# Optimization experiments

Hardware: AMD Instinct MI355X
Metric: run time of the kernel (lower is better)

The kernel has to match this reference:

```python
import jax, jax.numpy as jnp
import numpy as np

NPRE = 8        # diffusion iterations (production default 8000; math identical per step)
DEPS = 0.1
LAMBDA = 0.24
K_PM = 0.03     # exp(log(0.03)) buffer in the 'none' branch
ALPHA = 0.7
SIGMA_FREQ = 0.1


def _g_pm(x, K):
    # Perona-Malik conductance g(x) = 1 / (1 + |x^2| / K^2)
    return 1.0 / (1.0 + jnp.abs(x * x) / (K * K))


def _gaussian_blur3(x, sigma):
    # Replicates torch create_gaussian_kernel(3, sigma): linspace(-3//2, 3//2, 3) = [-2, -0.5, 1]
    xs = jnp.linspace(-2.0, 1.0, 3)
    g1 = jnp.exp(-(xs ** 2) / (2.0 * sigma * sigma))
    g1 = g1 / g1.sum()
    k2 = jnp.outer(g1, g1).astype(x.dtype)            # [3,3]
    C = x.shape[1]
    k = jnp.broadcast_to(k2, (C, 1, 3, 3))
    xp = jnp.pad(x, ((0, 0), (0, 0), (1, 1), (1, 1)), mode='reflect')
    return jax.lax.conv_general_dilated(
        xp, k, window_strides=(1, 1), padding='VALID',
        dimension_numbers=('NCHW', 'OIHW', 'NCHW'), feature_group_count=C)


def _edge_coeffs(I, K):
    # c(I): FFT high-pass edge response + finite differences -> Perona-Malik coefficients
    b, c_, h, w = I.shape
    F = jnp.fft.fft2(I, norm='ortho')
    y = jnp.linspace(-1.0, 1.0, h)[:, None]
    xg = jnp.linspace(-1.0, 1.0, w)[None, :]
    hf_mask = (jnp.sqrt(xg * xg + y * y) > 0.5).astype(I.dtype)   # [h,w]
    er = jnp.real(jnp.fft.ifft2(F * hf_mask, norm='ortho'))
    dv = jnp.abs(I[:, :, 1:, :] - I[:, :, :-1, :]) + er[:, :, 1:, :]
    dh = jnp.abs(I[:, :, :, 1:] - I[:, :, :, :-1]) + er[:, :, :, 1:]
    cv = _g_pm(jnp.mean(dv, axis=1, keepdims=True), K)   # [b,1,h-1,w]
    ch = _g_pm(jnp.mean(dh, axis=1, keepdims=True), K)   # [b,1,h,w-1]
    return cv, ch


def _diffuse_step(cv, ch, I, l=LAMBDA):
    # frequency-domain smoothing branch
    Ff = jnp.fft.fft2(I, norm='ortho')
    sr = _gaussian_blur3(jnp.real(Ff), SIGMA_FREQ)
    si = _gaussian_blur3(jnp.imag(Ff), SIGMA_FREQ)
    I_freq = jnp.real(jnp.fft.ifft2(jax.lax.complex(sr, si), norm='ortho'))
    dv = I[:, :, 1:, :] - I[:, :, :-1, :]
    dh = I[:, :, :, 1:] - I[:, :, :, :-1]
    I = ALPHA * I + (1.0 - ALPHA) * I_freq
    tv = l * cv * dv
    th = l * ch * dh
    I = I.at[:, :, 1:, :].add(-tv).at[:, :, :-1, :].add(tv)
    I = I.at[:, :, :, 1:].add(-th).at[:, :, :, :-1].add(th)
    return I


def _adjust_step(img, source, mask_inv, eps=1e-8):
    b, c_, h, w = img.shape
    sh, sw = source.shape[2], source.shape[3]
    fh, fw = h // sh, w // sw
    # AdaptiveAvgPool2d((sh,sw)) with integer factor == block mean
    img_ss = img.reshape(b, c_, sh, fh, sw, fw).mean(axis=(3, 5))
    ratio_ss = jnp.where(mask_inv, jnp.ones_like(img_ss), source / (img_ss + eps))
    # nearest upsample with integer factor == repeat
    ratio = jnp.repeat(jnp.repeat(ratio_ss, fh, axis=2), fw, axis=3)
    return img * ratio


def setup_inputs() -> dict:
    key = jax.random.key(0)
    k1, k2, k3, k4 = jax.random.split(key, 4)
    guide = jax.random.normal(k1, (4, 3, 1024, 1024), dtype=jnp.float32)
    source = jax.random.uniform(k2, (4, 1, 128, 128), dtype=jnp.float32)
    mask_lr = jax.random.uniform(k3, (4, 1, 128, 128), dtype=jnp.float32)
    y_bicubic = jax.random.uniform(k4, (4, 1, 1024, 1024), dtype=jnp.float32)
    return {"guide": guide, "source": source, "mask_lr": mask_lr, "y_bicubic": y_bicubic}


def reference(guide, source, mask_lr, y_bicubic):
    # depth shift when source.min() <= deps (uniform[0,1) source -> effectively always)
    shift = jnp.where(jnp.min(source) <= DEPS, DEPS, 0.0).astype(source.dtype)
    source = source + shift
    img = y_bicubic + shift
    mask_inv = mask_lr < 0.5

    # 'none' feature extractor: guide_feats = cat([guide, img], 1) -> [B,4,H,W]
    feats = jnp.concatenate([guide, img], axis=1)
    cv, ch = _edge_coeffs(feats, K_PM)

    def step(I, _):
        I = _diffuse_step(cv, ch, I)
        I = _adjust_step(I, source, mask_inv)
        return I, None

    img, _ = jax.lax.scan(step, img, None, length=NPRE)
    return img - shift
```

## Files before the change

kernel.cpp:

```cpp
#include <hip/hip_runtime.h>
#include <hip/hip_fp16.h>

namespace {

constexpr int H = 1024, W = 1024, NB = 4;
constexpr int SH = 128, SW = 128;
constexpr float LAM = 0.24f;
constexpr float KK = 0.03f * 0.03f;
constexpr float DEPS_V = 0.1f;
constexpr float FFT_SCALE = 1.0f / (1024.0f * 1024.0f);
constexpr int COL_LO = 256, NCOL = 512;

__device__ __forceinline__ float2 cadd(float2 a, float2 b) { return make_float2(a.x + b.x, a.y + b.y); }
__device__ __forceinline__ float2 csub(float2 a, float2 b) { return make_float2(a.x - b.x, a.y - b.y); }
__device__ __forceinline__ float2 cmul(float2 a, float2 b) {
  return make_float2(a.x * b.x - a.y * b.y, a.x * b.y + a.y * b.x);
}
__device__ __forceinline__ int phys2(int e) { return e + (e >> 4); }

__device__ __forceinline__ float shift_from_bits(const unsigned* minp) {
  float mn = __uint_as_float(minp[0]);
  return (mn <= DEPS_V) ? DEPS_V : 0.0f;
}

__global__ void k_shift_min(const float* __restrict__ src, unsigned* __restrict__ minp) {
  int t = threadIdx.x;
  int b0 = blockIdx.x * 1024;
  float m = fminf(fminf(src[b0 + t], src[b0 + t + 256]),
                  fminf(src[b0 + t + 512], src[b0 + t + 768]));
  for (int o = 32; o > 0; o >>= 1) m = fminf(m, __shfl_xor(m, o));
  __shared__ float sm[4];
  if ((t & 63) == 0) sm[t >> 6] = m;
  __syncthreads();
  if (t == 0) {
    float mm = fminf(fminf(sm[0], sm[1]), fminf(sm[2], sm[3]));
    atomicMin(minp, __float_as_uint(mm));
  }
}

template <int NS, bool INV>
__device__ __forceinline__ void r4_butterfly(float2 v[4], int j, float2 r[4]) {
  if (NS > 1) {
    int p = j & (NS - 1);
    float sn, cs;
    sincospif((INV ? 1.0f : -1.0f) * (float)p * (1.0f / (float)(2 * NS)), &sn, &cs);
    float2 w1 = make_float2(cs, sn);
    float2 w2 = cmul(w1, w1);
    float2 w3 = cmul(w2, w1);
    v[1] = cmul(v[1], w1);
    v[2] = cmul(v[2], w2);
    v[3] = cmul(v[3], w3);
  }
  float2 a0 = cadd(v[0], v[2]), a2 = csub(v[0], v[2]);
  float2 a1 = cadd(v[1], v[3]), a3 = csub(v[1], v[3]);
  a3 = INV ? make_float2(-a3.y, a3.x) : make_float2(a3.y, -a3.x);
  r[0] = cadd(a0, a1);
  r[2] = csub(a0, a1);
  r[1] = cadd(a2, a3);
  r[3] = csub(a2, a3);
}

template <int NS, bool INV>
__device__ __forceinline__ void r4_stage_lds(float2 v[4], float2* dst, int j) {
  float2 r[4];
  r4_butterfly<NS, INV>(v, j, r);
  int p = j & (NS - 1);
  int base = ((j - p) << 2) + p;
#pragma unroll
  for (int k = 0; k < 4; ++k) dst[phys2(base + k * NS)] = r[k];
}

__device__ __forceinline__ void lds_load4(const float2* src, float2 v[4], int j) {
#pragma unroll
  for (int k = 0; k < 4; ++k) v[k] = src[phys2(j + k * 256)];
}

template <bool INV>
__device__ void fft1024(float2 v[4], float2* b0, float2* b1, int j) {
  r4_stage_lds<1, INV>(v, b0, j);
  __syncthreads();
  lds_load4(b0, v, j);
  r4_stage_lds<4, INV>(v, b1, j);
  __syncthreads();
  lds_load4(b1, v, j);
  r4_stage_lds<16, INV>(v, b0, j);
  __syncthreads();
  lds_load4(b0, v, j);
  r4_stage_lds<64, INV>(v, b1, j);
  __syncthreads();
  lds_load4(b1, v, j);
  float2 r[4];
  r4_butterfly<256, INV>(v, j, r);
#pragma unroll
  for (int k = 0; k < 4; ++k) v[k] = r[k];
}

__global__ void k_rowfft_fwd(const float* __restrict__ guide, const float* __restrict__ ybic,
                             const unsigned* __restrict__ minp, float2* __restrict__ A) {
  __shared__ float2 b0[1088], b1[1088];
  int b = blockIdx.y, y0 = blockIdx.x * 2, j = threadIdx.x;
  float sh = shift_from_bits(minp);
  const float* g0 = guide + ((size_t)(b * 3 + 0) * H + y0) * W;
  const float* g1 = guide + ((size_t)(b * 3 + 1) * H + y0) * W;
  const float* g2 = guide + ((size_t)(b * 3 + 2) * H + y0) * W;
  const float* yb = ybic + ((size_t)b * H + y0) * W;
  float2 v[4];
#pragma unroll
  for (int k = 0; k < 4; ++k) {
    int x = j + k * 256;
    float s0 = g0[x] + g1[x] + g2[x] + (yb[x] + sh);
    float s1 = g0[x + W] + g1[x + W] + g2[x + W] + (yb[x + W] + sh);
    v[k] = make_float2(s0, s1);
  }
  fft1024<false>(v, b0, b1, j);
#pragma unroll
  for (int k = 0; k < 4; ++k) b0[phys2(j + k * 256)] = v[k];
  __syncthreads();
  float2* o0 = A + ((size_t)b * H + y0) * W;
  float2* o1 = o0 + W;
#pragma unroll
  for (int k = 0; k < 4; ++k) {
    int m = j + k * 256;
    float2 Zm = v[k];
    float2 Zc = b0[phys2((1024 - m) & 1023)];
    o0[m] = make_float2(0.5f * (Zm.x + Zc.x), 0.5f * (Zm.y - Zc.y));
    o1[m] = make_float2(0.5f * (Zm.y + Zc.y), 0.5f * (Zc.x - Zm.x));
  }
}

__global__ void k_transpose_fwd(const float2* __restrict__ A, float2* __restrict__ Bc) {
  __shared__ float2 tile[32][33];
  int b = blockIdx.z;
  int c0 = blockIdx.x * 32, y0 = blockIdx.y * 32;
  const float2* ip = A + (size_t)b * H * W;
  float2* op = Bc + (size_t)b * NCOL * H;
#pragma unroll
  for (int k = 0; k < 4; ++k)
    tile[threadIdx.y + k * 8][threadIdx.x] =
        ip[(size_t)(y0 + threadIdx.y + k * 8) * W + (COL_LO + c0 + threadIdx.x)];
  __syncthreads();
#pragma unroll
  for (int k = 0; k < 4; ++k)
    op[(size_t)(c0 + threadIdx.y + k * 8) * H + (y0 + threadIdx.x)] =
        tile[threadIdx.x][threadIdx.y + k * 8];
}

__global__ void k_transpose_bwd(const float2* __restrict__ Bc, float2* __restrict__ A) {
  __shared__ float2 tile[32][33];
  int b = blockIdx.z;
  int c0 = blockIdx.x * 32, y0 = blockIdx.y * 32;
  const float2* ip = Bc + (size_t)b * NCOL * H;
  float2* op = A + (size_t)b * H * W;
#pragma unroll
  for (int k = 0; k < 4; ++k)
    tile[threadIdx.y + k * 8][threadIdx.x] =
        ip[(size_t)(c0 + threadIdx.y + k * 8) * H + (y0 + threadIdx.x)];
  __syncthreads();
#pragma unroll
  for (int k = 0; k < 4; ++k)
    op[(size_t)(y0 + threadIdx.y + k * 8) * W + (COL_LO + c0 + threadIdx.x)] =
        tile[threadIdx.x][threadIdx.y + k * 8];
}

__global__ void k_colfft_mask(float2* __restrict__ Bc) {
  __shared__ float2 b0[1088], b1[1088];
  int b = blockIdx.y, r = blockIdx.x, j = threadIdx.x;
  int k2 = COL_LO + r;
  double xj = -1.0 + 2.0 * (double)k2 / 1023.0;
  double xj2 = xj * xj;
  float2* row = Bc + ((size_t)b * NCOL + r) * H;
  float2 v[4];
#pragma unroll
  for (int k = 0; k < 4; ++k) v[k] = row[j + k * 256];
  fft1024<false>(v, b0, b1, j);
#pragma unroll
  for (int k = 0; k < 4; ++k) {
    int i = j + k * 256;
    double yv = -1.0 + 2.0 * (double)i / 1023.0;
    if (xj2 + yv * yv <= 0.25) v[k] = make_float2(0.0f, 0.0f);
  }
  fft1024<true>(v, b0, b1, j);
#pragma unroll
  for (int k = 0; k < 4; ++k) row[j + k * 256] = v[k];
}

__global__ void k_rowfft_inv(const float2* __restrict__ A, float* __restrict__ er) {
  __shared__ float2 b0[1088], b1[1088];
  int b = blockIdx.y, y = blockIdx.x, j = threadIdx.x;
  const float2* in = A + ((size_t)b * H + y) * W;
  float2 v[4];
#pragma unroll
  for (int k = 0; k < 4; ++k) v[k] = in[j + k * 256];
  v[0].x *= 1024.0f; v[0].y *= 1024.0f;
  v[3].x *= 1024.0f; v[3].y *= 1024.0f;
  fft1024<true>(v, b0, b1, j);
  float* out = er + ((size_t)b * H + y) * W;
#pragma unroll
  for (int k = 0; k < 4; ++k) out[j + k * 256] = v[k].x * FFT_SCALE;
}

__global__ void k_coeffs(const float* __restrict__ guide, const float* __restrict__ ybic,
                         const float* __restrict__ er, __half2* __restrict__ cvh) {
  int b = blockIdx.y, y = blockIdx.x, t = threadIdx.x;
  int x0 = t * 4;
  const float* g = guide + (size_t)b * 3 * H * W;
  const float* yb = ybic + (size_t)b * H * W;
  const float* e = er + (size_t)b * H * W;
  __half2* cp = cvh + (size_t)b * H * W;
  const size_t CH = (size_t)H * W;
  size_t row = (size_t)y * W + x0;
  float4 a0 = *(const float4*)(g + row);
  float4 a1 = *(const float4*)(g + CH + row);
  float4 a2 = *(const float4*)(g + 2 * CH + row);
  float4 a3 = *(const float4*)(yb + row);
  float4 e0 = *(const float4*)(e + row);
  float A0[5] = {a0.x, a0.y, a0.z, a0.w, 0.f};
  float A1[5] = {a1.x, a1.y, a1.z, a1.w, 0.f};
  float A2[5] = {a2.x, a2.y, a2.z, a2.w, 0.f};
  float A3[5] = {a3.x, a3.y, a3.z, a3.w, 0.f};
  float E0[5] = {e0.x, e0.y, e0.z, e0.w, 0.f};
  bool hasR = (x0 + 4 < W);
  if (hasR) {
    A0[4] = g[row + 4]; A1[4] = g[CH + row + 4]; A2[4] = g[2 * CH + row + 4];
    A3[4] = yb[row + 4]; E0[4] = e[row + 4];
  }
  float B0[4], B1[4], B2[4], B3[4], E1[4];
  bool hasD = (y < H - 1);
  if (hasD) {
    float4 q0 = *(const float4*)(g + row + W);
    float4 q1 = *(const float4*)(g + CH + row + W);
    float4 q2 = *(const float4*)(g + 2 * CH + row + W);
    float4 q3 = *(const float4*)(yb + row + W);
    float4 q4 = *(const float4*)(e + row + W);
    B0[0]=q0.x; B0[1]=q0.y; B0[2]=q0.z; B0[3]=q0.w;
    B1[0]=q1.x; B1[1]=q1.y; B1[2]=q1.z; B1[3]=q1.w;
    B2[0]=q2.x; B2[1]=q2.y; B2[2]=q2.z; B2[3]=q2.w;
    B3[0]=q3.x; B3[1]=q3.y; B3[2]=q3.z; B3[3]=q3.w;
    E1[0]=q4.x; E1[1]=q4.y; E1[2]=q4.z; E1[3]=q4.w;
  }
  __half2 outq[4];
#pragma unroll
  for (int i = 0; i < 4; ++i) {
    float cvv = 0.0f;
    if (hasD) {
      float s = fabsf(B0[i] - A0[i]) + fabsf(B1[i] - A1[i]) +
                fabsf(B2[i] - A2[i]) + fabsf(B3[i] - A3[i]);
      s = (s + E1[i]) * 0.25f;
      cvv = 1.0f / (1.0f + (s * s) / KK);
    }
    float chv = 0.0f;
    if (i < 3 || hasR) {
      float s = fabsf(A0[i + 1] - A0[i]) + fabsf(A1[i + 1] - A1[i]) +
                fabsf(A2[i + 1] - A2[i]) + fabsf(A3[i + 1] - A3[i]);
      s = (s + E0[i + 1]) * 0.25f;
      chv = 1.0f / (1.0f + (s * s) / KK);
    }
    outq[i] = __floats2half2_rn(cvv, chv);
  }
  *(float4*)(cp + row) = *(const float4*)outq;
}

__device__ __forceinline__ void load8h(const __half* p, float o[8]) {
  float4 raw = *(const float4*)p;
  const __half2* h = (const __half2*)&raw;
#pragma unroll
  for (int i = 0; i < 4; ++i) {
    float2 f = __half22float2(h[i]);
    o[2 * i] = f.x; o[2 * i + 1] = f.y;
  }
}
__device__ __forceinline__ void load8f(const float* p, float o[8]) {
  float4 a = *(const float4*)p;
  float4 c = *(const float4*)(p + 4);
  o[0]=a.x; o[1]=a.y; o[2]=a.z; o[3]=a.w; o[4]=c.x; o[5]=c.y; o[6]=c.z; o[7]=c.w;
}
__device__ __forceinline__ void store8h(__half* p, const float o[8]) {
  float4 raw;
  __half2* h = (__half2*)&raw;
#pragma unroll
  for (int i = 0; i < 4; ++i) h[i] = __floats2half2_rn(o[2 * i], o[2 * i + 1]);
  *(float4*)p = raw;
}

template <bool FIRST, bool FINAL>
__global__ void k_diffuse_ratio(const float* __restrict__ inF, const __half* __restrict__ inH,
                                const float* __restrict__ ratio_in,
                                const unsigned* __restrict__ minp,
                                const __half2* __restrict__ cvh, const float* __restrict__ src,
                                const float* __restrict__ mask, float* __restrict__ outF,
                                __half* __restrict__ outH, float* __restrict__ ratio_out) {
  int b = blockIdx.z, tx = threadIdx.x, ty = threadIdx.y;
  int x0 = blockIdx.x * 256 + tx * 8;
  int y = blockIdx.y * 8 + ty;
  float sh = shift_from_bits(minp);
  float addv = FIRST ? sh : 0.0f;
  size_t base = (size_t)b * H * W;
  size_t row = (size_t)y * W + x0;
  bool hasU = (y > 0), hasD = (y < H - 1);
  bool hasL = (x0 > 0), hasR = (x0 + 8 < W);
  int px = x0 >> 3;
  float rq = 1.f, rup = 1.f, rdn = 1.f, rlf = 1.f, rrt = 1.f;
  if (!FIRST) {
    const float* rb = ratio_in + (size_t)b * SH * SW;
    int py = y >> 3;
    rq = rb[py * SW + px];
    rup = hasU ? rb[((y - 1) >> 3) * SW + px] : 1.f;
    rdn = hasD ? rb[((y + 1) >> 3) * SW + px] : 1.f;
    rlf = hasL ? rb[py * SW + (px - 1)] : 1.f;
    rrt = hasR ? rb[py * SW + (px + 1)] : 1.f;
  }
  float C[8], U[8] = {0}, D[8] = {0};
  float lf = 0.f, rt = 0.f;
  if (FIRST) {
    const float* I = inF + base;
    load8f(I + row, C);
    if (hasU) load8f(I + row - W, U);
    if (hasD) load8f(I + row + W, D);
    if (hasL) lf = I[row - 1];
    if (hasR) rt = I[row + 8];
  } else {
    const __half* I = inH + base;
    load8h(I + row, C);
    if (hasU) load8h(I + row - W, U);
    if (hasD) load8h(I + row + W, D);
    if (hasL) lf = __half2float(I[row - 1]);
    if (hasR) rt = __half2float(I[row + 8]);
  }
#pragma unroll
  for (int i = 0; i < 8; ++i) {
    C[i] = (C[i] + addv) * rq;
    U[i] = (U[i] + addv) * rup;
    D[i] = (D[i] + addv) * rdn;
  }
  lf = (lf + addv) * rlf;
  rt = (rt + addv) * rrt;
  const __half2* cp = cvh + base;
  float cvq[8], chq[8], cvu[8] = {0};
  {
    float4 r0 = *(const float4*)(cp + row);
    float4 r1 = *(const float4*)(cp + row + 4);
    const __half2* h0 = (const __half2*)&r0;
    const __half2* h1 = (const __half2*)&r1;
#pragma unroll
    for (int i = 0; i < 4; ++i) {
      float2 f = __half22float2(h0[i]); cvq[i] = f.x; chq[i] = f.y;
      float2 g = __half22float2(h1[i]); cvq[i + 4] = g.x; chq[i + 4] = g.y;
    }
    if (hasU) {
      float4 u0 = *(const float4*)(cp + row - W);
      float4 u1 = *(const float4*)(cp + row - W + 4);
      const __half2* p0 = (const __half2*)&u0;
      const __half2* p1 = (const __half2*)&u1;
#pragma unroll
      for (int i = 0; i < 4; ++i) {
        cvu[i] = __half2float(p0[i].x);
        cvu[i + 4] = __half2float(p1[i].x);
      }
    }
  }
  float chl = hasL ? __half2float(cp[row - 1].y) : 0.f;
  float acc[8];
#pragma unroll
  for (int i = 0; i < 8; ++i) {
    float L = (i == 0) ? lf : C[i - 1];
    float R = (i == 7) ? rt : C[i + 1];
    float cL = (i == 0) ? chl : chq[i - 1];
    float a = C[i];
    if (hasD) a += LAM * cvq[i] * (D[i] - C[i]);
    if (hasU) a -= LAM * cvu[i] * (C[i] - U[i]);
    if (i < 7 || hasR) a += LAM * chq[i] * (R - C[i]);
    if (i > 0 || hasL) a -= LAM * cL * (C[i] - L);
    acc[i] = a;
  }
  __shared__ float sd[8][32];
  __shared__ float rblk[32];
  sd[ty][tx] = acc[0] + acc[1] + acc[2] + acc[3] + acc[4] + acc[5] + acc[6] + acc[7];
  __syncthreads();
  if (ty == 0) {
    float s = 0.f;
#pragma unroll
    for (int r = 0; r < 8; ++r) s += sd[r][tx];
    size_t si = ((size_t)b * SH + blockIdx.y) * SW + (blockIdx.x * 32 + tx);
    float mean = s * (1.0f / 64.0f);
    float rv = (mask[si] < 0.5f) ? 1.0f : (src[si] + sh) / (mean + 1e-8f);
    if (FINAL) rblk[tx] = rv;
    else ratio_out[si] = rv;
  }
  if (FINAL) {
    __syncthreads();
    float rv = rblk[tx];
    float o[8];
#pragma unroll
    for (int i = 0; i < 8; ++i) o[i] = acc[i] * rv - sh;
    float* op = outF + base + row;
    *(float4*)op = make_float4(o[0], o[1], o[2], o[3]);
    *(float4*)(op + 4) = make_float4(o[4], o[5], o[6], o[7]);
  } else {
    store8h(outH + base + row, acc);
  }
}

}

extern "C" void kernel_launch(void* const* d_in, const int* in_sizes, int n_in, void* d_out,
                              int out_size, void* d_ws, size_t ws_size, hipStream_t stream) {
  (void)in_sizes; (void)n_in; (void)out_size; (void)ws_size;
  const float* guide = (const float*)d_in[0];
  const float* source = (const float*)d_in[1];
  const float* mask = (const float*)d_in[2];
  const float* ybic = (const float*)d_in[3];
  float* out = (float*)d_out;

  char* ws = (char*)d_ws;
  float2* A = (float2*)ws;
  float2* Bc = (float2*)(ws + (size_t)32 * 1024 * 1024);
  float* er = (float*)(ws + (size_t)32 * 1024 * 1024);
  __half2* cvh = (__half2*)(ws + (size_t)48 * 1024 * 1024);
  __half* hA = (__half*)ws;
  __half* hB = (__half*)(ws + (size_t)8 * 1024 * 1024);
  unsigned* minp = (unsigned*)(ws + (size_t)64 * 1024 * 1024);
  float* ratioA = (float*)(ws + (size_t)64 * 1024 * 1024 + 4096);
  float* ratioB = ratioA + (size_t)NB * SH * SW;

  k_shift_min<<<64, 256, 0, stream>>>(source, minp);

  k_rowfft_fwd<<<dim3(H / 2, NB), 256, 0, stream>>>(guide, ybic, minp, A);
  dim3 gT(NCOL / 32, H / 32, NB), bT(32, 8);
  k_transpose_fwd<<<gT, bT, 0, stream>>>(A, Bc);
  k_colfft_mask<<<dim3(NCOL, NB), 256, 0, stream>>>(Bc);
  k_transpose_bwd<<<gT, bT, 0, stream>>>(Bc, A);
  k_rowfft_inv<<<dim3(H, NB), 256, 0, stream>>>(A, er);

  k_coeffs<<<dim3(H, NB), 256, 0, stream>>>(guide, ybic, er, cvh);

  dim3 gD(W / 256, H / 8, NB), bD(32, 8);
  k_diffuse_ratio<true, false><<<gD, bD, 0, stream>>>(ybic, nullptr, nullptr, minp, cvh,
                                                      source, mask, nullptr, hA, ratioA);
  k_diffuse_ratio<false, false><<<gD, bD, 0, stream>>>(nullptr, hA, ratioA, minp, cvh,
                                                       source, mask, nullptr, hB, ratioB);
  k_diffuse_ratio<false, false><<<gD, bD, 0, stream>>>(nullptr, hB, ratioB, minp, cvh,
                                                       source, mask, nullptr, hA, ratioA);
  k_diffuse_ratio<false, false><<<gD, bD, 0, stream>>>(nullptr, hA, ratioA, minp, cvh,
                                                       source, mask, nullptr, hB, ratioB);
  k_diffuse_ratio<false, false><<<gD, bD, 0, stream>>>(nullptr, hB, ratioB, minp, cvh,
                                                       source, mask, nullptr, hA, ratioA);
  k_diffuse_ratio<false, false><<<gD, bD, 0, stream>>>(nullptr, hA, ratioA, minp, cvh,
                                                       source, mask, nullptr, hB, ratioB);
  k_diffuse_ratio<false, false><<<gD, bD, 0, stream>>>(nullptr, hB, ratioB, minp, cvh,
                                                       source, mask, nullptr, hA, ratioA);
  k_diffuse_ratio<false, true><<<gD, bD, 0, stream>>>(nullptr, hA, ratioA, minp, cvh,
                                                      source, mask, out, nullptr, ratioB);
}
```

Measured before the change: 306.8 us.

## Fuse two diffusion steps per kernel with shared-memory halo tiles

Replaces eight single-step diffusion launches with four launches that each run two steps. Each block loads a 16-row tile plus halo of the image and coefficients into LDS, computes the first step and its ratio over the halo region, then computes the second step from LDS. This halves global round trips of the half-precision image and coefficients and the launch count, at the cost of redundant halo compute, heavy LDS use and more synchronization. LAMBDA is also folded into the stored coefficients.

```diff
diff --git a/kernel.cpp b/kernel.cpp
--- a/kernel.cpp
+++ b/kernel.cpp
@@ -246,22 +246,22 @@
       float s = fabsf(B0[i] - A0[i]) + fabsf(B1[i] - A1[i]) +
                 fabsf(B2[i] - A2[i]) + fabsf(B3[i] - A3[i]);
       s = (s + E1[i]) * 0.25f;
-      cvv = 1.0f / (1.0f + (s * s) / KK);
+      cvv = LAM / (1.0f + (s * s) / KK);
     }
     float chv = 0.0f;
     if (i < 3 || hasR) {
       float s = fabsf(A0[i + 1] - A0[i]) + fabsf(A1[i + 1] - A1[i]) +
                 fabsf(A2[i + 1] - A2[i]) + fabsf(A3[i + 1] - A3[i]);
       s = (s + E0[i + 1]) * 0.25f;
-      chv = 1.0f / (1.0f + (s * s) / KK);
+      chv = LAM / (1.0f + (s * s) / KK);
     }
     outq[i] = __floats2half2_rn(cvv, chv);
   }
   *(float4*)(cp + row) = *(const float4*)outq;
 }
 
-__device__ __forceinline__ void load8h(const __half* p, float o[8]) {
-  float4 raw = *(const float4*)p;
+__device__ __forceinline__ void ld8(const __half* p, int c0, float o[8]) {
+  float4 raw = *(const float4*)(p + c0);
   const __half2* h = (const __half2*)&raw;
 #pragma unroll
   for (int i = 0; i < 4; ++i) {
@@ -269,134 +269,214 @@
     o[2 * i] = f.x; o[2 * i + 1] = f.y;
   }
 }
-__device__ __forceinline__ void load8f(const float* p, float o[8]) {
-  float4 a = *(const float4*)p;
-  float4 c = *(const float4*)(p + 4);
-  o[0]=a.x; o[1]=a.y; o[2]=a.z; o[3]=a.w; o[4]=c.x; o[5]=c.y; o[6]=c.z; o[7]=c.w;
-}
-__device__ __forceinline__ void store8h(__half* p, const float o[8]) {
+__device__ __forceinline__ void st8(__half* p, int c0, const float v[8]) {
   float4 raw;
   __half2* h = (__half2*)&raw;
 #pragma unroll
-  for (int i = 0; i < 4; ++i) h[i] = __floats2half2_rn(o[2 * i], o[2 * i + 1]);
-  *(float4*)p = raw;
-}
-
-template <bool FIRST, bool FINAL>
-__global__ void k_diffuse_ratio(const float* __restrict__ inF, const __half* __restrict__ inH,
-                                const float* __restrict__ ratio_in,
-                                const unsigned* __restrict__ minp,
-                                const __half2* __restrict__ cvh, const float* __restrict__ src,
-                                const float* __restrict__ mask, float* __restrict__ outF,
-                                __half* __restrict__ outH, float* __restrict__ ratio_out) {
-  int b = blockIdx.z, tx = threadIdx.x, ty = threadIdx.y;
-  int x0 = blockIdx.x * 256 + tx * 8;
-  int y = blockIdx.y * 8 + ty;
+  for (int i = 0; i < 4; ++i) h[i] = __floats2half2_rn(v[2 * i], v[2 * i + 1]);
+  *(float4*)(p + c0) = raw;
+}
+
+template <bool FIRST, bool LAST>
+__global__ __launch_bounds__(256, 2) void k_diffuse_pair(
+    const float* __restrict__ ybic, const __half* __restrict__ imgIn,
+    const float* __restrict__ ratio_in, const unsigned* __restrict__ minp,
+    const __half2* __restrict__ cvh, const float* __restrict__ src,
+    const float* __restrict__ mask, __half* __restrict__ imgOut,
+    float* __restrict__ ratio_out, float* __restrict__ out) {
+  __shared__ __align__(16) __half sImg[34 * 288];
+  __shared__ __align__(16) __half sCv[33 * 288];
+  __shared__ __align__(16) __half sCh[32 * 288];
+  __shared__ __align__(16) __half sAcc[32 * 288];
+  __shared__ float sSum[32][34];
+  __shared__ float sRatA[4][34];
+  __shared__ float sRatB[2][32];
+  __shared__ float sRin[6][36];
+
+  int bx = blockIdx.x, by = blockIdx.y, b = blockIdx.z;
+  int tx = threadIdx.x, ty = threadIdx.y;
+  int tid = ty * 32 + tx;
+  int x0 = bx * 256, y0 = by * 16;
   float sh = shift_from_bits(minp);
-  float addv = FIRST ? sh : 0.0f;
   size_t base = (size_t)b * H * W;
-  size_t row = (size_t)y * W + x0;
-  bool hasU = (y > 0), hasD = (y < H - 1);
-  bool hasL = (x0 > 0), hasR = (x0 + 8 < W);
-  int px = x0 >> 3;
-  float rq = 1.f, rup = 1.f, rdn = 1.f, rlf = 1.f, rrt = 1.f;
+
   if (!FIRST) {
-    const float* rb = ratio_in + (size_t)b * SH * SW;
-    int py = y >> 3;
-    rq = rb[py * SW + px];
-    rup = hasU ? rb[((y - 1) >> 3) * SW + px] : 1.f;
-    rdn = hasD ? rb[((y + 1) >> 3) * SW + px] : 1.f;
-    rlf = hasL ? rb[py * SW + (px - 1)] : 1.f;
-    rrt = hasR ? rb[py * SW + (px + 1)] : 1.f;
-  }
-  float C[8], U[8] = {0}, D[8] = {0};
-  float lf = 0.f, rt = 0.f;
-  if (FIRST) {
-    const float* I = inF + base;
-    load8f(I + row, C);
-    if (hasU) load8f(I + row - W, U);
-    if (hasD) load8f(I + row + W, D);
-    if (hasL) lf = I[row - 1];
-    if (hasR) rt = I[row + 8];
-  } else {
-    const __half* I = inH + base;
-    load8h(I + row, C);
-    if (hasU) load8h(I + row - W, U);
-    if (hasD) load8h(I + row + W, D);
-    if (hasL) lf = __half2float(I[row - 1]);
-    if (hasR) rt = __half2float(I[row + 8]);
-  }
-#pragma unroll
-  for (int i = 0; i < 8; ++i) {
-    C[i] = (C[i] + addv) * rq;
-    U[i] = (U[i] + addv) * rup;
-    D[i] = (D[i] + addv) * rdn;
-  }
-  lf = (lf + addv) * rlf;
-  rt = (rt + addv) * rrt;
-  const __half2* cp = cvh + base;
-  float cvq[8], chq[8], cvu[8] = {0};
-  {
-    float4 r0 = *(const float4*)(cp + row);
-    float4 r1 = *(const float4*)(cp + row + 4);
-    const __half2* h0 = (const __half2*)&r0;
-    const __half2* h1 = (const __half2*)&r1;
-#pragma unroll
-    for (int i = 0; i < 4; ++i) {
-      float2 f = __half22float2(h0[i]); cvq[i] = f.x; chq[i] = f.y;
-      float2 g = __half22float2(h1[i]); cvq[i + 4] = g.x; chq[i + 4] = g.y;
-    }
-    if (hasU) {
-      float4 u0 = *(const float4*)(cp + row - W);
-      float4 u1 = *(const float4*)(cp + row - W + 4);
-      const __half2* p0 = (const __half2*)&u0;
-      const __half2* p1 = (const __half2*)&u1;
+    if (tid < 216) {
+      int pr = tid / 36, pc = tid % 36;
+      int prg = 2 * by - 2 + pr, pcg = 32 * bx - 2 + pc;
+      float rv = 1.f;
+      if (prg >= 0 && prg < SH && pcg >= 0 && pcg < SW)
+        rv = ratio_in[((size_t)b * SH + prg) * SW + pcg];
+      sRin[pr][pc] = rv;
+    }
+    __syncthreads();
+  }
+
+  for (int e = ty; e < 34; e += 8) {
+    int yg = y0 - 9 + e;
+    bool yok = (yg >= 0 && yg < H);
+    for (int o = tx; o < 36; o += 32) {
+      int colg = x0 - 16 + 8 * o;
+      bool xok = (colg >= 0 && colg + 7 < W);
+      int c0 = 8 * o;
+      float4 packed = make_float4(0.f, 0.f, 0.f, 0.f);
+      if (yok && xok) {
+        if (FIRST) {
+          const float* p = ybic + base + (size_t)yg * W + colg;
+          float4 a = *(const float4*)p, c = *(const float4*)(p + 4);
+          __half2* hh = (__half2*)&packed;
+          hh[0] = __floats2half2_rn(a.x + sh, a.y + sh);
+          hh[1] = __floats2half2_rn(a.z + sh, a.w + sh);
+          hh[2] = __floats2half2_rn(c.x + sh, c.y + sh);
+          hh[3] = __floats2half2_rn(c.z + sh, c.w + sh);
+        } else {
+          float4 raw = *(const float4*)(imgIn + base + (size_t)yg * W + colg);
+          float r = sRin[((7 + e) >> 3)][o];
+          const __half2* hh = (const __half2*)&raw;
+          __half2* po = (__half2*)&packed;
+#pragma unroll
+          for (int i = 0; i < 4; ++i) {
+            float2 f = __half22float2(hh[i]);
+            po[i] = __floats2half2_rn(f.x * r, f.y * r);
+          }
+        }
+      }
+      *(float4*)&sImg[e * 288 + c0] = packed;
+      float4 cp0 = make_float4(0.f, 0.f, 0.f, 0.f), cp1 = cp0;
+      if (yok && xok) {
+        const __half2* p = cvh + base + (size_t)yg * W + colg;
+        cp0 = *(const float4*)p;
+        cp1 = *(const float4*)(p + 4);
+      }
+      __half cvs[8], chs[8];
+      const __half2* q0 = (const __half2*)&cp0;
+      const __half2* q1 = (const __half2*)&cp1;
 #pragma unroll
       for (int i = 0; i < 4; ++i) {
-        cvu[i] = __half2float(p0[i].x);
-        cvu[i + 4] = __half2float(p1[i].x);
+        cvs[i] = q0[i].x; chs[i] = q0[i].y;
+        cvs[4 + i] = q1[i].x; chs[4 + i] = q1[i].y;
       }
-    }
-  }
-  float chl = hasL ? __half2float(cp[row - 1].y) : 0.f;
-  float acc[8];
-#pragma unroll
-  for (int i = 0; i < 8; ++i) {
-    float L = (i == 0) ? lf : C[i - 1];
-    float R = (i == 7) ? rt : C[i + 1];
-    float cL = (i == 0) ? chl : chq[i - 1];
-    float a = C[i];
-    if (hasD) a += LAM * cvq[i] * (D[i] - C[i]);
-    if (hasU) a -= LAM * cvu[i] * (C[i] - U[i]);
-    if (i < 7 || hasR) a += LAM * chq[i] * (R - C[i]);
-    if (i > 0 || hasL) a -= LAM * cL * (C[i] - L);
-    acc[i] = a;
-  }
-  __shared__ float sd[8][32];
-  __shared__ float rblk[32];
-  sd[ty][tx] = acc[0] + acc[1] + acc[2] + acc[3] + acc[4] + acc[5] + acc[6] + acc[7];
-  __syncthreads();
-  if (ty == 0) {
+      if (e < 33) *(float4*)&sCv[e * 288 + c0] = *(const float4*)cvs;
+      if (e >= 1) *(float4*)&sCh[(e - 1) * 288 + c0] = *(const float4*)chs;
+    }
+  }
+  __syncthreads();
+
+  for (int rg = 0; rg < 4; ++rg) {
+    int em = rg * 8 + ty;
+    int e = em + 1;
+    const __half* rowC = &sImg[e * 288];
+    const __half* rowU = &sImg[(e - 1) * 288];
+    const __half* rowD = &sImg[(e + 1) * 288];
+    const __half* cvC = &sCv[e * 288];
+    const __half* cvU = &sCv[(e - 1) * 288];
+    const __half* chC = &sCh[em * 288];
+    for (int o = 1 + tx; o < 35; o += 32) {
+      int c0 = 8 * o;
+      float C[8], U[8], D[8], cvd[8], cvu[8], chr[8];
+      ld8(rowC, c0, C); ld8(rowU, c0, U); ld8(rowD, c0, D);
+      ld8(cvC, c0, cvd); ld8(cvU, c0, cvu); ld8(chC, c0, chr);
+      float L = __half2float(rowC[c0 - 1]);
+      float R = __half2float(rowC[c0 + 8]);
+      float chl = __half2float(chC[c0 - 1]);
+      float acc[8], s = 0.f;
+#pragma unroll
+      for (int i = 0; i < 8; ++i) {
+        float l = (i == 0) ? L : C[i - 1];
+        float r = (i == 7) ? R : C[i + 1];
+        float cl = (i == 0) ? chl : chr[i - 1];
+        float a = C[i] + cvd[i] * (D[i] - C[i]) - cvu[i] * (C[i] - U[i]) +
+                  chr[i] * (r - C[i]) - cl * (C[i] - l);
+        acc[i] = a;
+        s += a;
+      }
+      st8(&sAcc[em * 288], c0, acc);
+      sSum[em][o - 1] = s;
+    }
+  }
+  __syncthreads();
+
+  if (tid < 136) {
+    int pr = tid / 34, pc = tid % 34;
     float s = 0.f;
 #pragma unroll
-    for (int r = 0; r < 8; ++r) s += sd[r][tx];
-    size_t si = ((size_t)b * SH + blockIdx.y) * SW + (blockIdx.x * 32 + tx);
-    float mean = s * (1.0f / 64.0f);
-    float rv = (mask[si] < 0.5f) ? 1.0f : (src[si] + sh) / (mean + 1e-8f);
-    if (FINAL) rblk[tx] = rv;
-    else ratio_out[si] = rv;
-  }
-  if (FINAL) {
-    __syncthreads();
-    float rv = rblk[tx];
-    float o[8];
-#pragma unroll
-    for (int i = 0; i < 8; ++i) o[i] = acc[i] * rv - sh;
-    float* op = outF + base + row;
-    *(float4*)op = make_float4(o[0], o[1], o[2], o[3]);
-    *(float4*)(op + 4) = make_float4(o[4], o[5], o[6], o[7]);
-  } else {
-    store8h(outH + base + row, acc);
+    for (int r = 0; r < 8; ++r) s += sSum[pr * 8 + r][pc];
+    int prg = 2 * by - 1 + pr, pcg = 32 * bx - 1 + pc;
+    float rv = 1.f;
+    if (prg >= 0 && prg < SH && pcg >= 0 && pcg < SW) {
+      size_t si = ((size_t)b * SH + prg) * SW + pcg;
+      if (mask[si] >= 0.5f) rv = (src[si] + sh) / (s * (1.0f / 64.0f) + 1e-8f);
+    }
+    sRatA[pr][pc] = rv;
+  }
+  __syncthreads();
+
+  float accB[2][8];
+#pragma unroll
+  for (int hf = 0; hf < 2; ++hf) {
+    int tr = hf * 8 + ty;
+    int em = tr + 8, e = em + 1;
+    int o = 2 + tx, c0 = 8 * o;
+    const __half* rowC = &sAcc[em * 288];
+    const __half* rowU = &sAcc[(em - 1) * 288];
+    const __half* rowD = &sAcc[(em + 1) * 288];
+    const __half* cvC = &sCv[e * 288];
+    const __half* cvU = &sCv[(e - 1) * 288];
+    const __half* chC = &sCh[em * 288];
+    float rC = sRatA[1 + (tr >> 3)][1 + tx];
+    float rU = sRatA[(tr + 7) >> 3][1 + tx];
+    float rDn = sRatA[((tr + 1) >> 3) + 1][1 + tx];
+    float rL = sRatA[1 + (tr >> 3)][tx];
+    float rR = sRatA[1 + (tr >> 3)][tx + 2];
+    float C[8], U[8], D[8], cvd[8], cvu[8], chr[8];
+    ld8(rowC, c0, C); ld8(rowU, c0, U); ld8(rowD, c0, D);
+    ld8(cvC, c0, cvd); ld8(cvU, c0, cvu); ld8(chC, c0, chr);
+#pragma unroll
+    for (int i = 0; i < 8; ++i) { C[i] *= rC; U[i] *= rU; D[i] *= rDn; }
+    float L = __half2float(rowC[c0 - 1]) * rL;
+    float R = __half2float(rowC[c0 + 8]) * rR;
+    float chl = __half2float(chC[c0 - 1]);
+    float s = 0.f;
+#pragma unroll
+    for (int i = 0; i < 8; ++i) {
+      float l = (i == 0) ? L : C[i - 1];
+      float r = (i == 7) ? R : C[i + 1];
+      float cl = (i == 0) ? chl : chr[i - 1];
+      float a = C[i] + cvd[i] * (D[i] - C[i]) - cvu[i] * (C[i] - U[i]) +
+                chr[i] * (r - C[i]) - cl * (C[i] - l);
+      accB[hf][i] = a;
+      s += a;
+    }
+    sSum[tr][tx] = s;
+  }
+  __syncthreads();
+
+  if (tid < 64) {
+    int pr = tid >> 5, pc = tid & 31;
+    float s = 0.f;
+#pragma unroll
+    for (int r = 0; r < 8; ++r) s += sSum[pr * 8 + r][pc];
+    size_t si = ((size_t)b * SH + 2 * by + pr) * SW + (32 * bx + pc);
+    float rv = (mask[si] < 0.5f) ? 1.f : (src[si] + sh) / (s * (1.0f / 64.0f) + 1e-8f);
+    sRatB[pr][pc] = rv;
+    if (!LAST) ratio_out[si] = rv;
+  }
+  if (LAST) __syncthreads();
+
+#pragma unroll
+  for (int hf = 0; hf < 2; ++hf) {
+    int tr = hf * 8 + ty;
+    int yg = y0 + tr, colg = x0 + 8 * tx;
+    if (LAST) {
+      float rv = sRatB[tr >> 3][tx];
+      float* op = out + base + (size_t)yg * W + colg;
+      *(float4*)op = make_float4(accB[hf][0] * rv - sh, accB[hf][1] * rv - sh,
+                                 accB[hf][2] * rv - sh, accB[hf][3] * rv - sh);
+      *(float4*)(op + 4) = make_float4(accB[hf][4] * rv - sh, accB[hf][5] * rv - sh,
+                                       accB[hf][6] * rv - sh, accB[hf][7] * rv - sh);
+    } else {
+      st8(imgOut + base + (size_t)yg * W, colg, accB[hf]);
+    }
   }
 }
 
@@ -416,11 +496,11 @@
   float2* Bc = (float2*)(ws + (size_t)32 * 1024 * 1024);
   float* er = (float*)(ws + (size_t)32 * 1024 * 1024);
   __half2* cvh = (__half2*)(ws + (size_t)48 * 1024 * 1024);
-  __half* hA = (__half*)ws;
-  __half* hB = (__half*)(ws + (size_t)8 * 1024 * 1024);
+  __half* hA = (__half*)(ws + (size_t)8 * 1024 * 1024);
+  __half* hB = (__half*)(ws + (size_t)16 * 1024 * 1024);
   unsigned* minp = (unsigned*)(ws + (size_t)64 * 1024 * 1024);
-  float* ratioA = (float*)(ws + (size_t)64 * 1024 * 1024 + 4096);
-  float* ratioB = ratioA + (size_t)NB * SH * SW;
+  float* ratA = (float*)(ws + (size_t)64 * 1024 * 1024 + 4096);
+  float* ratB = ratA + (size_t)NB * SH * SW;
 
   k_shift_min<<<64, 256, 0, stream>>>(source, minp);
 
@@ -433,21 +513,13 @@
 
   k_coeffs<<<dim3(H, NB), 256, 0, stream>>>(guide, ybic, er, cvh);
 
-  dim3 gD(W / 256, H / 8, NB), bD(32, 8);
-  k_diffuse_ratio<true, false><<<gD, bD, 0, stream>>>(ybic, nullptr, nullptr, minp, cvh,
-                                                      source, mask, nullptr, hA, ratioA);
-  k_diffuse_ratio<false, false><<<gD, bD, 0, stream>>>(nullptr, hA, ratioA, minp, cvh,
-                                                       source, mask, nullptr, hB, ratioB);
-  k_diffuse_ratio<false, false><<<gD, bD, 0, stream>>>(nullptr, hB, ratioB, minp, cvh,
-                                                       source, mask, nullptr, hA, ratioA);
-  k_diffuse_ratio<false, false><<<gD, bD, 0, stream>>>(nullptr, hA, ratioA, minp, cvh,
-                                                       source, mask, nullptr, hB, ratioB);
-  k_diffuse_ratio<false, false><<<gD, bD, 0, stream>>>(nullptr, hB, ratioB, minp, cvh,
-                                                       source, mask, nullptr, hA, ratioA);
-  k_diffuse_ratio<false, false><<<gD, bD, 0, stream>>>(nullptr, hA, ratioA, minp, cvh,
-                                                       source, mask, nullptr, hB, ratioB);
-  k_diffuse_ratio<false, false><<<gD, bD, 0, stream>>>(nullptr, hB, ratioB, minp, cvh,
-                                                       source, mask, nullptr, hA, ratioA);
-  k_diffuse_ratio<false, true><<<gD, bD, 0, stream>>>(nullptr, hA, ratioA, minp, cvh,
-                                                      source, mask, out, nullptr, ratioB);
-}
+  dim3 gP(4, 64, NB), bP(32, 8);
+  k_diffuse_pair<true, false><<<gP, bP, 0, stream>>>(ybic, nullptr, nullptr, minp, cvh,
+                                                     source, mask, hA, ratA, nullptr);
+  k_diffuse_pair<false, false><<<gP, bP, 0, stream>>>(nullptr, hA, ratA, minp, cvh,
+                                                      source, mask, hB, ratB, nullptr);
+  k_diffuse_pair<false, false><<<gP, bP, 0, stream>>>(nullptr, hB, ratB, minp, cvh,
+                                                      source, mask, hA, ratA, nullptr);
+  k_diffuse_pair<false, true><<<gP, bP, 0, stream>>>(nullptr, hA, ratA, minp, cvh,
+                                                     source, mask, nullptr, nullptr, out);
+}
```

Result: no change. 307.3 us (+0.2%).
